# Kernel tuning notes

Hardware: AMD Instinct MI355X
Metric: run time of the kernel (lower is better)

## Reference

```python
import jax, jax.numpy as jnp
import numpy as np

# Quantum circuits here are products of single-qubit gates (no entanglement),
# so PauliZ expectations have closed forms:
#   attention head (RX(x) then trainable RX(theta)):  <Z> = cos(x + theta)
#   ffn qlayer    (RX(x) then trainable RY(phi)):     <Z> = cos(x) * cos(phi)

LN_EPS = 1e-5

def layernorm(x, g, b):
    mu = jnp.mean(x, axis=-1, keepdims=True)
    var = jnp.mean((x - mu) ** 2, axis=-1, keepdims=True)
    return (x - mu) * jax.lax.rsqrt(var + LN_EPS) * g + b

def sinusoidal_pe(S, E):
    pos = jnp.arange(S, dtype=jnp.float32)[:, None]
    div = jnp.exp(jnp.arange(0, E, 2, dtype=jnp.float32) * (-np.log(10000.0) / E))
    pe = jnp.zeros((S, E), dtype=jnp.float32)
    pe = pe.at[:, 0::2].set(jnp.sin(pos * div))
    pe = pe.at[:, 1::2].set(jnp.cos(pos * div))
    return pe

def setup_inputs() -> dict:
    key = jax.random.key(0)
    V, E, H, L, F, C, NQ = 32000, 512, 128, 6, 2048, 10, 4
    B, S = 8, 2048
    ks = jax.random.split(key, 16)
    s = 0.02
    return {
        "tokens": jax.random.randint(ks[0], (B, S), 0, V, dtype=jnp.int32),
        "emb": jax.random.normal(ks[1], (V, E), jnp.float32) * s,
        "theta_attn": jax.random.normal(ks[2], (L, H, NQ), jnp.float32),
        "combine_W": jax.random.normal(ks[3], (L, E, E), jnp.float32) * s,
        "combine_b": jnp.zeros((L, E), jnp.float32),
        "ln1_g": jnp.ones((L, E), jnp.float32),
        "ln1_b": jnp.zeros((L, E), jnp.float32),
        "phi_ffn": jax.random.normal(ks[4], (L, NQ), jnp.float32),
        "lin1_W": jax.random.normal(ks[5], (L, F, NQ), jnp.float32) * s,
        "lin1_b": jnp.zeros((L, F), jnp.float32),
        "lin2_W": jax.random.normal(ks[6], (L, E, F), jnp.float32) * s,
        "lin2_b": jnp.zeros((L, E), jnp.float32),
        "ln2_g": jnp.ones((L, E), jnp.float32),
        "ln2_b": jnp.zeros((L, E), jnp.float32),
        "cls_W": jax.random.normal(ks[7], (C, E), jnp.float32) * s,
        "cls_b": jnp.zeros((C,), jnp.float32),
    }

def reference(tokens, emb, theta_attn, combine_W, combine_b, ln1_g, ln1_b,
              phi_ffn, lin1_W, lin1_b, lin2_W, lin2_b, ln2_g, ln2_b,
              cls_W, cls_b):
    B, S = tokens.shape
    E = emb.shape[1]
    L, H, NQ = theta_attn.shape
    dk = E // H  # == NQ by construction
    x = emb[tokens] + sinusoidal_pe(S, E)[None]  # (B,S,E)
    nqf = phi_ffn.shape[1]
    for l in range(L):
        # quantum multi-head attention: per-token per-head <Z> = cos(x + theta)
        heads = x.reshape(B, S, H, dk)
        attn_q = jnp.cos(heads + theta_attn[l][None, None]).reshape(B, S, E)
        attn = jnp.einsum('bse,fe->bsf', attn_q, combine_W[l]) + combine_b[l]
        x = layernorm(x + attn, ln1_g[l], ln1_b[l])
        # quantum FFN: <Z> = cos(x_i) * cos(phi_i) on first nqf features
        z = jnp.cos(x[..., :nqf]) * jnp.cos(phi_ffn[l])  # (B,S,nqf)
        h = jax.nn.relu(jnp.einsum('bsq,fq->bsf', z, lin1_W[l]) + lin1_b[l])
        ffn = jnp.einsum('bsf,ef->bse', h, lin2_W[l]) + lin2_b[l]
        x = layernorm(x + ffn, ln2_g[l], ln2_b[l])
    pooled = jnp.mean(x, axis=1)  # (B,E) mean-pool over sequence
    return pooled @ cls_W.T + cls_b  # (B,C)
```

## Files before the change

kernel.cpp:

```cpp
#include <hip/hip_runtime.h>
#include <hip/hip_bf16.h>
#include <math.h>

#define LN_EPS 1e-5f

constexpr int Bb = 8, Ss = 2048, Ee = 512, Ll = 6, Ff = 2048, Cc = 10;
constexpr int Nn = Bb * Ss;

typedef __attribute__((ext_vector_type(8))) short short8v;
typedef __attribute__((ext_vector_type(4))) float f32x4;

__device__ __forceinline__ unsigned short f2bf(float f) {
    unsigned int b = __float_as_uint(f);
    b += 0x7FFFu + ((b >> 16) & 1u);
    return (unsigned short)(b >> 16);
}

__device__ __forceinline__ float fastcos(float x) {
    float r = x * 0.15915494309189535f;
    r = __builtin_amdgcn_fractf(r);
    return __builtin_amdgcn_cosf(r);
}

__device__ __forceinline__ void gload16(const void* g, void* lds) {
    __builtin_amdgcn_global_load_lds(
        (__attribute__((address_space(1))) void*)(g),
        (__attribute__((address_space(3))) void*)(lds),
        16, 0, 0);
}

__global__ void pe_kernel(float* __restrict__ pe) {
    int p = blockIdx.x * blockDim.x + threadIdx.x;
    int total = Ss * (Ee / 2);
    if (p >= total) return;
    int s = p / (Ee / 2);
    int i = p % (Ee / 2);
    float div = expf(float(2 * i) * (-logf(10000.0f) / float(Ee)));
    float ang = float(s) * div;
    pe[s * Ee + 2 * i]     = sinf(ang);
    pe[s * Ee + 2 * i + 1] = cosf(ang);
}

__global__ void embed_kernel(const int* __restrict__ tokens,
                             const float* __restrict__ emb,
                             const float* __restrict__ pe,
                             const float* __restrict__ theta0,
                             float* __restrict__ x,
                             unsigned short* __restrict__ acos) {
    int idx = blockIdx.x * blockDim.x + threadIdx.x;
    int total = Nn * Ee / 4;
    if (idx >= total) return;
    int n  = idx / (Ee / 4);
    int e4 = idx % (Ee / 4);
    int tok = tokens[n];
    int s = n % Ss;
    f32x4 a = *(const f32x4*)(emb + (size_t)tok * Ee + e4 * 4);
    f32x4 p = *(const f32x4*)(pe + (size_t)s * Ee + e4 * 4);
    f32x4 o = a + p;
    *(f32x4*)(x + (size_t)n * Ee + e4 * 4) = o;
    f32x4 t = *(const f32x4*)(theta0 + e4 * 4);
    ushort4 c;
    c.x = f2bf(fastcos(o.x + t.x));
    c.y = f2bf(fastcos(o.y + t.y));
    c.z = f2bf(fastcos(o.z + t.z));
    c.w = f2bf(fastcos(o.w + t.w));
    *(ushort4*)(acos + (size_t)n * Ee + e4 * 4) = c;
}

__global__ void cvt_bf16(const float* __restrict__ in,
                         unsigned short* __restrict__ out, int n4) {
    int i = blockIdx.x * blockDim.x + threadIdx.x;
    if (i >= n4) return;
    f32x4 v = *(const f32x4*)(in + (size_t)i * 4);
    ushort4 o;
    o.x = f2bf(v.x); o.y = f2bf(v.y); o.z = f2bf(v.z); o.w = f2bf(v.w);
    *(ushort4*)(out + (size_t)i * 4) = o;
}

__global__ __launch_bounds__(256) void h_kernel(const float* __restrict__ z,
                                                const float* __restrict__ W1,
                                                const float* __restrict__ b1,
                                                unsigned short* __restrict__ H) {
    __shared__ unsigned short hls[8 * Ff];
    const int t  = threadIdx.x;
    const int m0 = blockIdx.x * 8;
    f32x4 zr[8];
#pragma unroll
    for (int r = 0; r < 8; ++r)
        zr[r] = *(const f32x4*)(z + (size_t)(m0 + r) * 4);
#pragma unroll
    for (int j = 0; j < 8; ++j) {
        const int f = t + 256 * j;
        f32x4 w = *(const f32x4*)(W1 + (size_t)f * 4);
        float bb = b1[f];
#pragma unroll
        for (int r = 0; r < 8; ++r) {
            float v = zr[r].x * w.x + zr[r].y * w.y + zr[r].z * w.z +
                      zr[r].w * w.w + bb;
            hls[r * Ff + f] = f2bf(fmaxf(v, 0.f));
        }
    }
    __syncthreads();
#pragma unroll
    for (int j = 0; j < 8; ++j) {
        const int idx = (j * 256 + t) * 8;
        *(short8v*)(H + (size_t)m0 * Ff + idx) = *(const short8v*)(&hls[idx]);
    }
}

__global__ __launch_bounds__(256) void gemm_bf16(
    const unsigned short* __restrict__ A,
    const unsigned short* __restrict__ Wb,
    const float* __restrict__ bias,
    const float* __restrict__ xres,
    float* __restrict__ Cout,
    int K) {
    __shared__ unsigned short As[2][128 * 64];
    __shared__ unsigned short Bs[2][128 * 64];
    const int tid  = threadIdx.x;
    const int lane = tid & 63;
    const int wid  = tid >> 6;
    const int wr   = wid >> 1;
    const int wc   = wid & 1;
    const int row0 = blockIdx.x * 128;
    const int col0 = blockIdx.y * 128;
    const int srow   = lane >> 3;
    const int pchunk = lane & 7;

    f32x4 acc[4][4];
#pragma unroll
    for (int m = 0; m < 4; m++)
#pragma unroll
        for (int n = 0; n < 4; n++) acc[m][n] = {0.f, 0.f, 0.f, 0.f};

    const int NT = K >> 6;

    auto STAGE = [&](int buf, int k0) {
#pragma unroll
        for (int seg = 0; seg < 4; ++seg) {
            const int s   = wid * 4 + seg;
            const int row = s * 8 + srow;
            const int lc  = pchunk ^ (row & 7);
            gload16(A  + (size_t)(row0 + row) * K + k0 + lc * 8, &As[buf][s * 512]);
            gload16(Wb + (size_t)(col0 + row) * K + k0 + lc * 8, &Bs[buf][s * 512]);
        }
    };

    auto COMPUTE = [&](int buf) {
#pragma unroll
        for (int ks = 0; ks < 2; ks++) {
            const int k8 = ks * 4 + (lane >> 4);
            short8v aF[4], bF[4];
#pragma unroll
            for (int m = 0; m < 4; m++) {
                const int row = wr * 64 + m * 16 + (lane & 15);
                aF[m] = *(const short8v*)(&As[buf][row * 64 + ((k8 ^ (row & 7)) * 8)]);
            }
#pragma unroll
            for (int n = 0; n < 4; n++) {
                const int row = wc * 64 + n * 16 + (lane & 15);
                bF[n] = *(const short8v*)(&Bs[buf][row * 64 + ((k8 ^ (row & 7)) * 8)]);
            }
#pragma unroll
            for (int m = 0; m < 4; m++)
#pragma unroll
                for (int n = 0; n < 4; n++)
                    acc[m][n] = __builtin_amdgcn_mfma_f32_16x16x32_bf16(
                        aF[m], bF[n], acc[m][n], 0, 0, 0);
        }
    };

    STAGE(0, 0);
    int cur = 0;
    for (int kt = 0; kt < NT; ++kt) {
        if (kt + 1 < NT) {
            STAGE(cur ^ 1, (kt + 1) << 6);
            asm volatile("s_waitcnt vmcnt(8)" ::: "memory");
        } else {
            asm volatile("s_waitcnt vmcnt(0)" ::: "memory");
        }
        __builtin_amdgcn_s_barrier();
        asm volatile("" ::: "memory");
        COMPUTE(cur);
        asm volatile("" ::: "memory");
        __builtin_amdgcn_s_barrier();
        cur ^= 1;
    }

#pragma unroll
    for (int m = 0; m < 4; m++) {
#pragma unroll
        for (int n = 0; n < 4; n++) {
            int colg = col0 + wc * 64 + n * 16 + (lane & 15);
            float bv = bias[colg];
#pragma unroll
            for (int j = 0; j < 4; j++) {
                int rowg = row0 + wr * 64 + m * 16 + ((lane >> 4) * 4) + j;
                size_t off = (size_t)rowg * 512 + colg;
                Cout[off] = acc[m][n][j] + bv + xres[off];
            }
        }
    }
}

__global__ __launch_bounds__(256) void ln_fused(
    const float* __restrict__ tmp, float* __restrict__ x,
    const float* __restrict__ g, const float* __restrict__ b,
    const float* __restrict__ phi, float* __restrict__ z,
    const float* __restrict__ theta, unsigned short* __restrict__ acos) {
    const int row  = blockIdx.x * 4 + (threadIdx.x >> 6);
    const int lane = threadIdx.x & 63;
    const float* tr = tmp + (size_t)row * Ee;
    f32x4 v0 = *(const f32x4*)(tr + lane * 4);
    f32x4 v1 = *(const f32x4*)(tr + 256 + lane * 4);
    float s = v0.x + v0.y + v0.z + v0.w + v1.x + v1.y + v1.z + v1.w;
#pragma unroll
    for (int o = 32; o; o >>= 1) s += __shfl_xor(s, o);
    float mu = s * (1.f / 512.f);
    f32x4 d0 = {v0.x - mu, v0.y - mu, v0.z - mu, v0.w - mu};
    f32x4 d1 = {v1.x - mu, v1.y - mu, v1.z - mu, v1.w - mu};
    float q = d0.x * d0.x + d0.y * d0.y + d0.z * d0.z + d0.w * d0.w +
              d1.x * d1.x + d1.y * d1.y + d1.z * d1.z + d1.w * d1.w;
#pragma unroll
    for (int o = 32; o; o >>= 1) q += __shfl_xor(q, o);
    float rs = rsqrtf(q * (1.f / 512.f) + LN_EPS);
    f32x4 g0 = *(const f32x4*)(g + lane * 4);
    f32x4 b0 = *(const f32x4*)(b + lane * 4);
    f32x4 g1 = *(const f32x4*)(g + 256 + lane * 4);
    f32x4 b1v = *(const f32x4*)(b + 256 + lane * 4);
    f32x4 o0 = {d0.x * rs * g0.x + b0.x, d0.y * rs * g0.y + b0.y,
                d0.z * rs * g0.z + b0.z, d0.w * rs * g0.w + b0.w};
    f32x4 o1 = {d1.x * rs * g1.x + b1v.x, d1.y * rs * g1.y + b1v.y,
                d1.z * rs * g1.z + b1v.z, d1.w * rs * g1.w + b1v.w};
    *(f32x4*)(x + (size_t)row * Ee + lane * 4) = o0;
    *(f32x4*)(x + (size_t)row * Ee + 256 + lane * 4) = o1;
    if (z != nullptr && lane == 0) {
        z[(size_t)row * 4 + 0] = fastcos(o0.x) * fastcos(phi[0]);
        z[(size_t)row * 4 + 1] = fastcos(o0.y) * fastcos(phi[1]);
        z[(size_t)row * 4 + 2] = fastcos(o0.z) * fastcos(phi[2]);
        z[(size_t)row * 4 + 3] = fastcos(o0.w) * fastcos(phi[3]);
    }
    if (acos != nullptr) {
        f32x4 t0 = *(const f32x4*)(theta + lane * 4);
        f32x4 t1 = *(const f32x4*)(theta + 256 + lane * 4);
        ushort4 c0, c1;
        c0.x = f2bf(fastcos(o0.x + t0.x));
        c0.y = f2bf(fastcos(o0.y + t0.y));
        c0.z = f2bf(fastcos(o0.z + t0.z));
        c0.w = f2bf(fastcos(o0.w + t0.w));
        c1.x = f2bf(fastcos(o1.x + t1.x));
        c1.y = f2bf(fastcos(o1.y + t1.y));
        c1.z = f2bf(fastcos(o1.z + t1.z));
        c1.w = f2bf(fastcos(o1.w + t1.w));
        *(ushort4*)(acos + (size_t)row * Ee + lane * 4) = c0;
        *(ushort4*)(acos + (size_t)row * Ee + 256 + lane * 4) = c1;
    }
}

__global__ __launch_bounds__(256) void pool_part(const float* __restrict__ x,
                                                 float* __restrict__ part) {
    int bidx = blockIdx.x, ch = blockIdx.y;
    int t = threadIdx.x;
    float s0 = 0.f, s1 = 0.f;
    for (int s = 0; s < 64; ++s) {
        const float* row = x + ((size_t)bidx * Ss + ch * 64 + s) * Ee;
        s0 += row[t];
        s1 += row[t + 256];
    }
    float* pr = part + ((size_t)(bidx * 32 + ch)) * Ee;
    pr[t] = s0;
    pr[t + 256] = s1;
}

__global__ __launch_bounds__(256) void cls_kernel(const float* __restrict__ part,
                                                  const float* __restrict__ clsW,
                                                  const float* __restrict__ clsb,
                                                  float* __restrict__ out) {
    int bidx = blockIdx.x;
    int t = threadIdx.x;
    float p0 = 0.f, p1 = 0.f;
    for (int ch = 0; ch < 32; ++ch) {
        const float* pr = part + ((size_t)(bidx * 32 + ch)) * Ee;
        p0 += pr[t];
        p1 += pr[t + 256];
    }
    p0 *= (1.f / float(Ss));
    p1 *= (1.f / float(Ss));
    __shared__ float red[256];
    for (int c = 0; c < Cc; ++c) {
        red[t] = p0 * clsW[(size_t)c * Ee + t] + p1 * clsW[(size_t)c * Ee + t + 256];
        __syncthreads();
        for (int s2 = 128; s2 > 0; s2 >>= 1) {
            if (t < s2) red[t] += red[t + s2];
            __syncthreads();
        }
        if (t == 0) out[bidx * Cc + c] = red[0] + clsb[c];
        __syncthreads();
    }
}

extern "C" void kernel_launch(void* const* d_in, const int* in_sizes, int n_in,
                              void* d_out, int out_size, void* d_ws, size_t ws_size,
                              hipStream_t stream) {
    const int*   tokens     = (const int*)d_in[0];
    const float* emb        = (const float*)d_in[1];
    const float* theta_attn = (const float*)d_in[2];
    const float* combine_W  = (const float*)d_in[3];
    const float* combine_b  = (const float*)d_in[4];
    const float* ln1_g      = (const float*)d_in[5];
    const float* ln1_b      = (const float*)d_in[6];
    const float* phi_ffn    = (const float*)d_in[7];
    const float* lin1_W     = (const float*)d_in[8];
    const float* lin1_b     = (const float*)d_in[9];
    const float* lin2_W     = (const float*)d_in[10];
    const float* lin2_b     = (const float*)d_in[11];
    const float* ln2_g      = (const float*)d_in[12];
    const float* ln2_b      = (const float*)d_in[13];
    const float* cls_W      = (const float*)d_in[14];
    const float* cls_b      = (const float*)d_in[15];
    float* out = (float*)d_out;

    float* x    = (float*)d_ws;
    float* tmp  = x + (size_t)Nn * Ee;
    float* z    = tmp + (size_t)Nn * Ee;
    float* part = z + (size_t)Nn * 4;
    unsigned short* Wcb  = (unsigned short*)(part + (size_t)Bb * 32 * Ee);
    unsigned short* W2b  = Wcb + (size_t)Ll * Ee * Ee;
    unsigned short* acos = W2b + (size_t)Ll * Ee * Ff;
    unsigned short* H    = acos + (size_t)Nn * Ee;
    float* pe = (float*)H;

    {
        int total = Ss * (Ee / 2);
        pe_kernel<<<(total + 255) / 256, 256, 0, stream>>>(pe);
    }
    {
        int total = Nn * Ee / 4;
        embed_kernel<<<(total + 255) / 256, 256, 0, stream>>>(
            tokens, emb, pe, theta_attn, x, acos);
    }
    {
        int n4c = Ll * Ee * Ee / 4;
        cvt_bf16<<<(n4c + 255) / 256, 256, 0, stream>>>(combine_W, Wcb, n4c);
        int n42 = Ll * Ee * Ff / 4;
        cvt_bf16<<<(n42 + 255) / 256, 256, 0, stream>>>(lin2_W, W2b, n42);
    }

    dim3 ggrid(Nn / 128, Ee / 128);
    for (int l = 0; l < Ll; l++) {
        const unsigned short* cWl = Wcb + (size_t)l * Ee * Ee;
        const float* cbl  = combine_b + (size_t)l * Ee;
        const float* g1   = ln1_g + (size_t)l * Ee;
        const float* b1n  = ln1_b + (size_t)l * Ee;
        const float* phil = phi_ffn + (size_t)l * 4;
        const float* w1l  = lin1_W + (size_t)l * Ff * 4;
        const float* b1l  = lin1_b + (size_t)l * Ff;
        const unsigned short* w2l = W2b + (size_t)l * Ee * Ff;
        const float* b2l  = lin2_b + (size_t)l * Ee;
        const float* g2   = ln2_g + (size_t)l * Ee;
        const float* b2n  = ln2_b + (size_t)l * Ee;
        const float* thn  = (l + 1 < Ll) ? theta_attn + (size_t)(l + 1) * Ee : nullptr;
        unsigned short* acn = (l + 1 < Ll) ? acos : nullptr;

        gemm_bf16<<<ggrid, 256, 0, stream>>>(acos, cWl, cbl, x, tmp, Ee);
        ln_fused<<<Nn / 4, 256, 0, stream>>>(tmp, x, g1, b1n, phil, z,
                                             nullptr, nullptr);
        h_kernel<<<Nn / 8, 256, 0, stream>>>(z, w1l, b1l, H);
        gemm_bf16<<<ggrid, 256, 0, stream>>>(H, w2l, b2l, x, tmp, Ff);
        ln_fused<<<Nn / 4, 256, 0, stream>>>(tmp, x, g2, b2n, nullptr, nullptr,
                                             thn, acn);
    }

    pool_part<<<dim3(Bb, 32), 256, 0, stream>>>(x, part);
    cls_kernel<<<Bb, 256, 0, stream>>>(part, cls_W, cls_b, out);
}
```

Measured before the change: 655.7 us.

## Single-buffer GEMM LDS and remap workgroups for XCD-aware tile locality

Replaces the double-buffered LDS pipeline in the bf16 GEMM with a single buffer and plain barriers, halving LDS use to allow more resident workgroups. It also changes to a 1D grid with a swizzle that spreads consecutive block IDs across the 8 XCDs, so the four column tiles of the same row block land on the same XCD and share its L2. The cost is that global-load latency is no longer overlapped with MFMA compute inside a block and must be hidden by occupancy instead.

```diff
diff --git a/kernel.cpp b/kernel.cpp
--- a/kernel.cpp
+++ b/kernel.cpp
@@ -115,15 +115,17 @@
     const float* __restrict__ xres,
     float* __restrict__ Cout,
     int K) {
-    __shared__ unsigned short As[2][128 * 64];
-    __shared__ unsigned short Bs[2][128 * 64];
+    __shared__ unsigned short As[128 * 64];
+    __shared__ unsigned short Bs[128 * 64];
     const int tid  = threadIdx.x;
     const int lane = tid & 63;
     const int wid  = tid >> 6;
     const int wr   = wid >> 1;
     const int wc   = wid & 1;
-    const int row0 = blockIdx.x * 128;
-    const int col0 = blockIdx.y * 128;
+    const int wg   = blockIdx.x;
+    const int sw   = (wg & 7) * 64 + (wg >> 3);
+    const int row0 = (sw >> 2) * 128;
+    const int col0 = (sw & 3) * 128;
     const int srow   = lane >> 3;
     const int pchunk = lane & 7;
 
@@ -135,18 +137,18 @@
 
     const int NT = K >> 6;
 
-    auto STAGE = [&](int buf, int k0) {
+    auto STAGE = [&](int k0) {
 #pragma unroll
         for (int seg = 0; seg < 4; ++seg) {
             const int s   = wid * 4 + seg;
             const int row = s * 8 + srow;
             const int lc  = pchunk ^ (row & 7);
-            gload16(A  + (size_t)(row0 + row) * K + k0 + lc * 8, &As[buf][s * 512]);
-            gload16(Wb + (size_t)(col0 + row) * K + k0 + lc * 8, &Bs[buf][s * 512]);
+            gload16(A  + (size_t)(row0 + row) * K + k0 + lc * 8, &As[s * 512]);
+            gload16(Wb + (size_t)(col0 + row) * K + k0 + lc * 8, &Bs[s * 512]);
         }
     };
 
-    auto COMPUTE = [&](int buf) {
+    auto COMPUTE = [&]() {
 #pragma unroll
         for (int ks = 0; ks < 2; ks++) {
             const int k8 = ks * 4 + (lane >> 4);
@@ -154,12 +156,12 @@
 #pragma unroll
             for (int m = 0; m < 4; m++) {
                 const int row = wr * 64 + m * 16 + (lane & 15);
-                aF[m] = *(const short8v*)(&As[buf][row * 64 + ((k8 ^ (row & 7)) * 8)]);
+                aF[m] = *(const short8v*)(&As[row * 64 + ((k8 ^ (row & 7)) * 8)]);
             }
 #pragma unroll
             for (int n = 0; n < 4; n++) {
                 const int row = wc * 64 + n * 16 + (lane & 15);
-                bF[n] = *(const short8v*)(&Bs[buf][row * 64 + ((k8 ^ (row & 7)) * 8)]);
+                bF[n] = *(const short8v*)(&Bs[row * 64 + ((k8 ^ (row & 7)) * 8)]);
             }
 #pragma unroll
             for (int m = 0; m < 4; m++)
@@ -170,21 +172,11 @@
         }
     };
 
-    STAGE(0, 0);
-    int cur = 0;
     for (int kt = 0; kt < NT; ++kt) {
-        if (kt + 1 < NT) {
-            STAGE(cur ^ 1, (kt + 1) << 6);
-            asm volatile("s_waitcnt vmcnt(8)" ::: "memory");
-        } else {
-            asm volatile("s_waitcnt vmcnt(0)" ::: "memory");
-        }
-        __builtin_amdgcn_s_barrier();
-        asm volatile("" ::: "memory");
-        COMPUTE(cur);
-        asm volatile("" ::: "memory");
-        __builtin_amdgcn_s_barrier();
-        cur ^= 1;
+        STAGE(kt << 6);
+        __syncthreads();
+        COMPUTE();
+        __syncthreads();
     }
 
 #pragma unroll
@@ -346,7 +338,7 @@
         cvt_bf16<<<(n42 + 255) / 256, 256, 0, stream>>>(lin2_W, W2b, n42);
     }
 
-    dim3 ggrid(Nn / 128, Ee / 128);
+    const int ngemm = (Nn / 128) * (Ee / 128);
     for (int l = 0; l < Ll; l++) {
         const unsigned short* cWl = Wcb + (size_t)l * Ee * Ee;
         const float* cbl  = combine_b + (size_t)l * Ee;
@@ -362,11 +354,11 @@
         const float* thn  = (l + 1 < Ll) ? theta_attn + (size_t)(l + 1) * Ee : nullptr;
         unsigned short* acn = (l + 1 < Ll) ? acos : nullptr;
 
-        gemm_bf16<<<ggrid, 256, 0, stream>>>(acos, cWl, cbl, x, tmp, Ee);
+        gemm_bf16<<<ngemm, 256, 0, stream>>>(acos, cWl, cbl, x, tmp, Ee);
         ln_fused<<<Nn / 4, 256, 0, stream>>>(tmp, x, g1, b1n, phil, z,
                                              nullptr, nullptr);
         h_kernel<<<Nn / 8, 256, 0, stream>>>(z, w1l, b1l, H);
-        gemm_bf16<<<ggrid, 256, 0, stream>>>(H, w2l, b2l, x, tmp, Ff);
+        gemm_bf16<<<ngemm, 256, 0, stream>>>(H, w2l, b2l, x, tmp, Ff);
         ln_fused<<<Nn / 4, 256, 0, stream>>>(tmp, x, g2, b2n, nullptr, nullptr,
                                              thn, acn);
     }
```

Result: slower. 702.2 us (+7.1%).
